# Optimization experiments

Hardware: AMD Instinct MI355X
Metric: run time of the kernel (lower is better)

Reference implementation:

```python
import jax, jax.numpy as jnp
import numpy as np

B, HE, WE = 4, 256, 512      # batch, env-map height/width (lat-long)
N, S = 32, 128               # sampled env directions per iter, output image size
PIXELS = 8192                # segmentation pixel count (dataset constant)


def setup_inputs() -> dict:
    key = jax.random.key(0)
    ks = jax.random.split(key, 12)
    d = {}
    d["x"] = jax.random.uniform(ks[0], (B, HE, WE, 3), jnp.float32)
    d["y"] = jax.random.uniform(ks[1], (B, HE, WE, 3), jnp.float32)
    for i, base in ((0, 2), (1, 7)):
        d[f"brdfSpec_{i}"] = jax.random.uniform(ks[base], (N, 1, S, S), jnp.float32)
        d[f"brdfDiffuse_{i}"] = jax.random.uniform(ks[base + 1], (N, 1, S, S), jnp.float32)
        d[f"idx_{i}"] = jax.random.randint(ks[base + 2], (N, S, S), 0, WE, jnp.int32)
        d[f"idy_{i}"] = jax.random.randint(ks[base + 3], (N, S, S), 0, HE, jnp.int32)
        d[f"weight_{i}"] = jax.random.uniform(ks[base + 4], (N, 1), jnp.float32)
    return d


def _render_pass(env, brdf_spec, brdf_diff, idx, idy, weight):
    # env: [B,HE,WE,3]; idx/idy: [N,S,S]; brdf: [N,1,S,S]; weight: [N,1]
    g = env[:, idy, idx, :]                    # gather -> [B,N,S,S,3]
    g = jnp.transpose(g, (0, 1, 4, 2, 3))      # [B,N,3,S,S]
    w = weight[None, :, :, None, None]         # [1,N,1,1,1]
    diffuse = jnp.sum(brdf_diff[None] * w * g, axis=1)   # [B,3,S,S]
    spec = 10.0 * jnp.sum(brdf_spec[None] * w * g, axis=1)
    return diffuse + spec


def reference(x, y, brdfSpec_0, brdfDiffuse_0, idx_0, idy_0, weight_0,
              brdfSpec_1, brdfDiffuse_1, idx_1, idy_1, weight_1):
    pred = (_render_pass(x, brdfSpec_0, brdfDiffuse_0, idx_0, idy_0, weight_0)
            + _render_pass(x, brdfSpec_1, brdfDiffuse_1, idx_1, idy_1, weight_1))
    gt = (_render_pass(y, brdfSpec_0, brdfDiffuse_0, idx_0, idy_0, weight_0)
          + _render_pass(y, brdfSpec_1, brdfDiffuse_1, idx_1, idy_1, weight_1))
    pixel_num = PIXELS * x.shape[0] * 3
    loss = jnp.sum((pred - gt) ** 2) / pixel_num
    return (loss, pred[0], gt[0])
```

## Files before the change

kernel.cpp:

```cpp
#include <hip/hip_runtime.h>

#define HWE 131072
#define OPIX 16384

typedef float f32x2 __attribute__((ext_vector_type(2)));

__global__ __launch_bounds__(256) void k_repack1(
    const float* __restrict__ x, const float* __restrict__ y,
    uint4* __restrict__ env) {
  int px = blockIdx.x * 256 + threadIdx.x;
  float o[16];
  #pragma unroll
  for (int c = 0; c < 3; c++) {
    float x0 = x[(size_t)px * 3 + c];
    float y0 = y[(size_t)px * 3 + c];
    o[c]     = x0;
    o[3 + c] = y0;
    #pragma unroll
    for (int b = 1; b < 4; b++) {
      float xv = x[((size_t)b * HWE + px) * 3 + c];
      float yv = y[((size_t)b * HWE + px) * 3 + c];
      o[3 + b * 3 + c] = xv - yv;
    }
  }
  o[15] = 0.f;
  uint4 q;
  q.x = (unsigned)__builtin_amdgcn_cvt_pk_fp8_f32(o[2],  o[3],
        __builtin_amdgcn_cvt_pk_fp8_f32(o[0],  o[1],  0, false), true);
  q.y = (unsigned)__builtin_amdgcn_cvt_pk_fp8_f32(o[6],  o[7],
        __builtin_amdgcn_cvt_pk_fp8_f32(o[4],  o[5],  0, false), true);
  q.z = (unsigned)__builtin_amdgcn_cvt_pk_fp8_f32(o[10], o[11],
        __builtin_amdgcn_cvt_pk_fp8_f32(o[8],  o[9],  0, false), true);
  q.w = (unsigned)__builtin_amdgcn_cvt_pk_fp8_f32(o[14], o[15],
        __builtin_amdgcn_cvt_pk_fp8_f32(o[12], o[13], 0, false), true);
  env[px] = q;
}

#define SLAB 516
__global__ __launch_bounds__(512) void k_render_fused(
    const float* __restrict__ bs0, const float* __restrict__ bd0,
    const int* __restrict__ ix0, const int* __restrict__ iy0,
    const float* __restrict__ w0,
    const float* __restrict__ bs1, const float* __restrict__ bd1,
    const int* __restrict__ ix1, const int* __restrict__ iy1,
    const float* __restrict__ w1,
    const uint4* __restrict__ env, float* __restrict__ d_out,
    float* __restrict__ loss_part) {
  int tid = threadIdx.x;
  int g = tid >> 5;
  int opl = tid & 31;
  int opix = blockIdx.x * 32 + opl;

  const float* bs; const float* bd; const int* ix; const int* iy; const float* w;
  if (g < 8) { bs = bs0; bd = bd0; ix = ix0; iy = iy0; w = w0; }
  else       { bs = bs1; bd = bd1; ix = ix1; iy = iy1; w = w1; }
  int n0 = (g & 7) * 4;

  float acc[15];
  #pragma unroll
  for (int j = 0; j < 15; j++) acc[j] = 0.f;

  #pragma unroll
  for (int k = 0; k < 4; k++) {
    int n = n0 + k;
    int off = n * OPIX + opix;
    float coef = (bd[off] + 10.0f * bs[off]) * w[n];
    int gp = iy[off] * 512 + ix[off];
    uint4 q = env[gp];
    f32x2 v;
    v = __builtin_amdgcn_cvt_pk_f32_fp8(q.x, false); acc[0]  = fmaf(coef, v.x, acc[0]);  acc[1]  = fmaf(coef, v.y, acc[1]);
    v = __builtin_amdgcn_cvt_pk_f32_fp8(q.x, true);  acc[2]  = fmaf(coef, v.x, acc[2]);  acc[3]  = fmaf(coef, v.y, acc[3]);
    v = __builtin_amdgcn_cvt_pk_f32_fp8(q.y, false); acc[4]  = fmaf(coef, v.x, acc[4]);  acc[5]  = fmaf(coef, v.y, acc[5]);
    v = __builtin_amdgcn_cvt_pk_f32_fp8(q.y, true);  acc[6]  = fmaf(coef, v.x, acc[6]);  acc[7]  = fmaf(coef, v.y, acc[7]);
    v = __builtin_amdgcn_cvt_pk_f32_fp8(q.z, false); acc[8]  = fmaf(coef, v.x, acc[8]);  acc[9]  = fmaf(coef, v.y, acc[9]);
    v = __builtin_amdgcn_cvt_pk_f32_fp8(q.z, true);  acc[10] = fmaf(coef, v.x, acc[10]); acc[11] = fmaf(coef, v.y, acc[11]);
    v = __builtin_amdgcn_cvt_pk_f32_fp8(q.w, false); acc[12] = fmaf(coef, v.x, acc[12]); acc[13] = fmaf(coef, v.y, acc[13]);
    v = __builtin_amdgcn_cvt_pk_f32_fp8(q.w, true);  acc[14] = fmaf(coef, v.x, acc[14]);
  }

  __shared__ float sm[16 * SLAB];
  __shared__ float fin[32 * 17];
  {
    float4* my = (float4*)&sm[g * SLAB + opl * 16];
    my[0] = make_float4(acc[0],  acc[1],  acc[2],  acc[3]);
    my[1] = make_float4(acc[4],  acc[5],  acc[6],  acc[7]);
    my[2] = make_float4(acc[8],  acc[9],  acc[10], acc[11]);
    my[3] = make_float4(acc[12], acc[13], acc[14], 0.f);
  }
  __syncthreads();

  {
    int opl2 = tid >> 4;
    int cp = tid & 15;
    float s = 0.f;
    #pragma unroll
    for (int g2 = 0; g2 < 16; g2++)
      s += sm[g2 * SLAB + opl2 * 16 + cp];
    fin[opl2 * 17 + cp] = s;
  }
  __syncthreads();

  if (tid < 32) {
    float a[15];
    #pragma unroll
    for (int c = 0; c < 15; c++) a[c] = fin[tid * 17 + c];
    int op = blockIdx.x * 32 + tid;
    float l = 0.f;
    #pragma unroll
    for (int c = 0; c < 3; c++) {
      d_out[1 + c * OPIX + op]       = a[c];
      d_out[1 + (3 + c) * OPIX + op] = a[3 + c];
      float d0 = a[c] - a[3 + c];
      l += d0 * d0 + a[6 + c] * a[6 + c] + a[9 + c] * a[9 + c]
         + a[12 + c] * a[12 + c];
    }
    #pragma unroll
    for (int s = 16; s > 0; s >>= 1) l += __shfl_down(l, s);
    if (tid == 0) loss_part[blockIdx.x] = l;
  }
}

__global__ __launch_bounds__(256) void k_loss(
    const float* __restrict__ loss_part, float* __restrict__ d_out) {
  int tid = threadIdx.x;
  float v = loss_part[tid] + loss_part[tid + 256];
  #pragma unroll
  for (int s = 32; s > 0; s >>= 1) v += __shfl_down(v, s, 64);
  __shared__ float red[4];
  int lane = tid & 63, wid = tid >> 6;
  if (lane == 0) red[wid] = v;
  __syncthreads();
  if (tid == 0)
    d_out[0] = (red[0] + red[1] + red[2] + red[3]) * (1.0f / 98304.0f);
}

extern "C" void kernel_launch(void* const* d_in, const int* in_sizes, int n_in,
                              void* d_out, int out_size, void* d_ws, size_t ws_size,
                              hipStream_t stream) {
  const float* x   = (const float*)d_in[0];
  const float* y   = (const float*)d_in[1];
  const float* bs0 = (const float*)d_in[2];
  const float* bd0 = (const float*)d_in[3];
  const int*   ix0 = (const int*)  d_in[4];
  const int*   iy0 = (const int*)  d_in[5];
  const float* w0  = (const float*)d_in[6];
  const float* bs1 = (const float*)d_in[7];
  const float* bd1 = (const float*)d_in[8];
  const int*   ix1 = (const int*)  d_in[9];
  const int*   iy1 = (const int*)  d_in[10];
  const float* w1  = (const float*)d_in[11];
  float* out = (float*)d_out;

  uint4* env       = (uint4*)d_ws;
  float* loss_part = (float*)((char*)d_ws + (size_t)HWE * 16);

  hipLaunchKernelGGL(k_repack1, dim3(HWE / 256), dim3(256), 0, stream,
                     x, y, env);
  hipLaunchKernelGGL(k_render_fused, dim3(OPIX / 32), dim3(512), 0, stream,
                     bs0, bd0, ix0, iy0, w0, bs1, bd1, ix1, iy1, w1,
                     env, out, loss_part);
  hipLaunchKernelGGL(k_loss, dim3(1), dim3(256), 0, stream, loss_part, out);
}
```

Before: 21.09 us.

## Fuse loss reduction into render kernel via last-block atomic, halve pixels per block

Removes the separate single-block loss kernel by having each render block bump an atomic counter, with the last block reducing all partial losses. The counter is reset inside the repack kernel. The render kernel now covers 16 output pixels per block with 2 directions per group instead of 4, doubling the grid to give more parallelism, and it adds a launch-bounds occupancy hint. Input loads in the repack kernel become nontemporal. The cost is an atomic plus thread fences in every block, and more shared-memory reduction per output pixel.

```diff
diff --git a/kernel.cpp b/kernel.cpp
--- a/kernel.cpp
+++ b/kernel.cpp
@@ -7,19 +7,20 @@
 
 __global__ __launch_bounds__(256) void k_repack1(
     const float* __restrict__ x, const float* __restrict__ y,
-    uint4* __restrict__ env) {
+    uint4* __restrict__ env, unsigned* __restrict__ cnt) {
   int px = blockIdx.x * 256 + threadIdx.x;
+  if (blockIdx.x == 0 && threadIdx.x == 0) *cnt = 0;
   float o[16];
   #pragma unroll
   for (int c = 0; c < 3; c++) {
-    float x0 = x[(size_t)px * 3 + c];
-    float y0 = y[(size_t)px * 3 + c];
+    float x0 = __builtin_nontemporal_load(&x[(size_t)px * 3 + c]);
+    float y0 = __builtin_nontemporal_load(&y[(size_t)px * 3 + c]);
     o[c]     = x0;
     o[3 + c] = y0;
     #pragma unroll
     for (int b = 1; b < 4; b++) {
-      float xv = x[((size_t)b * HWE + px) * 3 + c];
-      float yv = y[((size_t)b * HWE + px) * 3 + c];
+      float xv = __builtin_nontemporal_load(&x[((size_t)b * HWE + px) * 3 + c]);
+      float yv = __builtin_nontemporal_load(&y[((size_t)b * HWE + px) * 3 + c]);
       o[3 + b * 3 + c] = xv - yv;
     }
   }
@@ -36,8 +37,8 @@
   env[px] = q;
 }
 
-#define SLAB 516
-__global__ __launch_bounds__(512) void k_render_fused(
+#define SLAB 260
+__global__ __launch_bounds__(512, 8) void k_render_fused(
     const float* __restrict__ bs0, const float* __restrict__ bd0,
     const int* __restrict__ ix0, const int* __restrict__ iy0,
     const float* __restrict__ w0,
@@ -45,23 +46,23 @@
     const int* __restrict__ ix1, const int* __restrict__ iy1,
     const float* __restrict__ w1,
     const uint4* __restrict__ env, float* __restrict__ d_out,
-    float* __restrict__ loss_part) {
+    float* __restrict__ loss_part, unsigned* __restrict__ cnt) {
   int tid = threadIdx.x;
-  int g = tid >> 5;
-  int opl = tid & 31;
-  int opix = blockIdx.x * 32 + opl;
+  int g = tid >> 4;
+  int opl = tid & 15;
+  int opix = blockIdx.x * 16 + opl;
 
   const float* bs; const float* bd; const int* ix; const int* iy; const float* w;
-  if (g < 8) { bs = bs0; bd = bd0; ix = ix0; iy = iy0; w = w0; }
-  else       { bs = bs1; bd = bd1; ix = ix1; iy = iy1; w = w1; }
-  int n0 = (g & 7) * 4;
+  if (g < 16) { bs = bs0; bd = bd0; ix = ix0; iy = iy0; w = w0; }
+  else        { bs = bs1; bd = bd1; ix = ix1; iy = iy1; w = w1; }
+  int n0 = (g & 15) * 2;
 
   float acc[15];
   #pragma unroll
   for (int j = 0; j < 15; j++) acc[j] = 0.f;
 
   #pragma unroll
-  for (int k = 0; k < 4; k++) {
+  for (int k = 0; k < 2; k++) {
     int n = n0 + k;
     int off = n * OPIX + opix;
     float coef = (bd[off] + 10.0f * bs[off]) * w[n];
@@ -78,8 +79,9 @@
     v = __builtin_amdgcn_cvt_pk_f32_fp8(q.w, true);  acc[14] = fmaf(coef, v.x, acc[14]);
   }
 
-  __shared__ float sm[16 * SLAB];
-  __shared__ float fin[32 * 17];
+  __shared__ float sm[32 * SLAB];
+  __shared__ float fin[16 * 17];
+  __shared__ int is_last;
   {
     float4* my = (float4*)&sm[g * SLAB + opl * 16];
     my[0] = make_float4(acc[0],  acc[1],  acc[2],  acc[3]);
@@ -89,22 +91,22 @@
   }
   __syncthreads();
 
-  {
-    int opl2 = tid >> 4;
+  if (tid < 256) {
+    int px = tid >> 4;
     int cp = tid & 15;
     float s = 0.f;
     #pragma unroll
-    for (int g2 = 0; g2 < 16; g2++)
-      s += sm[g2 * SLAB + opl2 * 16 + cp];
-    fin[opl2 * 17 + cp] = s;
+    for (int g2 = 0; g2 < 32; g2++)
+      s += sm[g2 * SLAB + px * 16 + cp];
+    fin[px * 17 + cp] = s;
   }
   __syncthreads();
 
-  if (tid < 32) {
+  if (tid < 16) {
     float a[15];
     #pragma unroll
     for (int c = 0; c < 15; c++) a[c] = fin[tid * 17 + c];
-    int op = blockIdx.x * 32 + tid;
+    int op = blockIdx.x * 16 + tid;
     float l = 0.f;
     #pragma unroll
     for (int c = 0; c < 3; c++) {
@@ -115,23 +117,33 @@
          + a[12 + c] * a[12 + c];
     }
     #pragma unroll
-    for (int s = 16; s > 0; s >>= 1) l += __shfl_down(l, s);
+    for (int s = 8; s > 0; s >>= 1) l += __shfl_down(l, s, 16);
     if (tid == 0) loss_part[blockIdx.x] = l;
   }
-}
 
-__global__ __launch_bounds__(256) void k_loss(
-    const float* __restrict__ loss_part, float* __restrict__ d_out) {
-  int tid = threadIdx.x;
-  float v = loss_part[tid] + loss_part[tid + 256];
-  #pragma unroll
-  for (int s = 32; s > 0; s >>= 1) v += __shfl_down(v, s, 64);
-  __shared__ float red[4];
-  int lane = tid & 63, wid = tid >> 6;
-  if (lane == 0) red[wid] = v;
+  if (tid == 0) {
+    __threadfence();
+    unsigned old = atomicAdd(cnt, 1u);
+    is_last = (old == gridDim.x - 1) ? 1 : 0;
+  }
   __syncthreads();
-  if (tid == 0)
-    d_out[0] = (red[0] + red[1] + red[2] + red[3]) * (1.0f / 98304.0f);
+  if (is_last) {
+    if (tid == 0) *cnt = 0;
+    __threadfence();
+    float v = loss_part[tid] + loss_part[tid + 512];
+    #pragma unroll
+    for (int s = 32; s > 0; s >>= 1) v += __shfl_down(v, s, 64);
+    __shared__ float red[8];
+    int lane = tid & 63, wid = tid >> 6;
+    if (lane == 0) red[wid] = v;
+    __syncthreads();
+    if (tid == 0) {
+      float t = 0.f;
+      #pragma unroll
+      for (int i = 0; i < 8; i++) t += red[i];
+      d_out[0] = t * (1.0f / 98304.0f);
+    }
+  }
 }
 
 extern "C" void kernel_launch(void* const* d_in, const int* in_sizes, int n_in,
@@ -151,13 +163,13 @@
   const float* w1  = (const float*)d_in[11];
   float* out = (float*)d_out;
 
-  uint4* env       = (uint4*)d_ws;
-  float* loss_part = (float*)((char*)d_ws + (size_t)HWE * 16);
+  uint4*    env       = (uint4*)d_ws;
+  float*    loss_part = (float*)((char*)d_ws + (size_t)HWE * 16);
+  unsigned* cnt       = (unsigned*)(loss_part + 1024);
 
   hipLaunchKernelGGL(k_repack1, dim3(HWE / 256), dim3(256), 0, stream,
-                     x, y, env);
-  hipLaunchKernelGGL(k_render_fused, dim3(OPIX / 32), dim3(512), 0, stream,
+                     x, y, env, cnt);
+  hipLaunchKernelGGL(k_render_fused, dim3(OPIX / 16), dim3(512), 0, stream,
                      bs0, bd0, ix0, iy0, w0, bs1, bd1, ix1, iy1, w1,
-                     env, out, loss_part);
-  hipLaunchKernelGGL(k_loss, dim3(1), dim3(256), 0, stream, loss_part, out);
+                     env, out, loss_part, cnt);
 }
```

Result: slower. 55.21 us (+161.8%).
